# Kernel tuning notes

Measured on AMD Instinct MI355X. Metric: run time of the kernel, lower is better.

Reference implementation:

```python
import jax, jax.numpy as jnp
import numpy as np

IN_SHAPE = (8, 8, 8, 8)   # prod = 4096 in_features
OUT_SHAPE = (8, 8, 8, 8)  # prod = 4096 out_features
RANKS = (1, 64, 64, 64, 1)


def mpo2matrix(cores):
    # cores[k]: (r_k, i_k, o_k, r_{k+1}); contract the TT chain over rank axes.
    t = cores[0]
    for c in cores[1:]:
        t = jnp.tensordot(t, c, axes=([-1], [0]))
    # t: (1, i1,o1, i2,o2, i3,o3, i4,o4, 1) -> drop boundary ranks
    n = len(IN_SHAPE)
    io = tuple(d for p in zip(IN_SHAPE, OUT_SHAPE) for d in p)
    t = t.reshape(io)  # (i1,o1,...,in,on)
    perm = tuple(range(1, 2 * n, 2)) + tuple(range(0, 2 * n, 2))  # outputs first
    t = jnp.transpose(t, perm)
    return t.reshape(int(np.prod(OUT_SHAPE)), int(np.prod(IN_SHAPE)))  # (O, I)


def setup_inputs() -> dict:
    key = jax.random.key(0)
    ks = jax.random.split(key, 6)
    scale = 0.05  # keep reconstructed weight well-conditioned
    cores = []
    for i in range(4):
        r0, r1 = RANKS[i], RANKS[i + 1]
        cores.append(scale * jax.random.normal(ks[i], (r0, IN_SHAPE[i], OUT_SHAPE[i], r1), dtype=jnp.float32))
    x = jax.random.normal(ks[4], (8, 2048, 4096), dtype=jnp.float32)
    bias = jnp.zeros((4096,), dtype=jnp.float32)
    return {"x": x, "core0": cores[0], "core1": cores[1], "core2": cores[2], "core3": cores[3], "bias": bias}


def reference(x, core0, core1, core2, core3, bias):
    W = mpo2matrix([core0, core1, core2, core3])  # (O, I)
    res = x.reshape(-1, x.shape[-1])              # (B*S, I)
    out = res @ W.T + bias                        # F.linear
    return out.reshape(x.shape[:-1] + (-1,))
```

## Files before the change

### kernel.cpp

```cpp
#include <hip/hip_runtime.h>
#include <hip/hip_bf16.h>
#include <stdint.h>

typedef unsigned short u16;
typedef __attribute__((ext_vector_type(4))) float f32x4;
typedef __attribute__((ext_vector_type(8))) __bf16 bf16x8;

#define K_DIM 4096

__device__ __forceinline__ u16 f2bf_rne(float f) {
  union { float f; uint32_t u; } v; v.f = f;
  uint32_t u = v.u;
  return (u16)((u + 0x7fffu + ((u >> 16) & 1u)) >> 16);
}

__device__ __forceinline__ void gld_lds16(const u16* g, u16* l) {
  __builtin_amdgcn_global_load_lds((const __attribute__((address_space(1))) void*)g,
                                   (__attribute__((address_space(3))) void*)l,
                                   16, 0, 0);
}

__global__ __launch_bounds__(256) void k_cvt_x(const float* __restrict__ x, u16* __restrict__ xb, int n4) {
  const int stride = gridDim.x * 256;
  for (int i = blockIdx.x * 256 + threadIdx.x; i < n4; i += stride) {
    f32x4 a = ((const f32x4*)x)[i];
    uint2 o;
    o.x = (uint32_t)f2bf_rne(a[0]) | ((uint32_t)f2bf_rne(a[1]) << 16);
    o.y = (uint32_t)f2bf_rne(a[2]) | ((uint32_t)f2bf_rne(a[3]) << 16);
    ((uint2*)xb)[i] = o;
  }
}

__global__ __launch_bounds__(256) void k_t1(const float* __restrict__ c0, const float* __restrict__ c1,
                                            float* __restrict__ T1) {
  const int col = blockIdx.x * 256 + threadIdx.x;
  const int row = blockIdx.y;
  float acc = 0.f;
#pragma unroll 16
  for (int r = 0; r < 64; ++r) acc += c0[row * 64 + r] * c1[(size_t)r * 4096 + col];
  T1[(size_t)row * 4096 + col] = acc;
}

__global__ __launch_bounds__(256) void k_t2(const float* __restrict__ T1, const float* __restrict__ c2,
                                            float* __restrict__ T2) {
  __shared__ float t1s[16][64];
  const int tid = threadIdx.x;
  const int rowbase = blockIdx.y * 16;
  for (int idx = tid; idx < 1024; idx += 256)
    t1s[idx >> 6][idx & 63] = T1[(size_t)(rowbase + (idx >> 6)) * 64 + (idx & 63)];
  __syncthreads();
  const int col = blockIdx.x * 256 + tid;
  float acc[16];
#pragma unroll
  for (int j = 0; j < 16; ++j) acc[j] = 0.f;
  for (int r = 0; r < 64; ++r) {
    float b = c2[(size_t)r * 4096 + col];
#pragma unroll
    for (int j = 0; j < 16; ++j) acc[j] += t1s[j][r] * b;
  }
#pragma unroll
  for (int j = 0; j < 16; ++j) T2[(size_t)(rowbase + j) * 4096 + col] = acc[j];
}

__global__ __launch_bounds__(256) void k_w(const float* __restrict__ T2, const float* __restrict__ c3,
                                           u16* __restrict__ Wb) {
  __shared__ float t2p[64 * 65];
  __shared__ float c3t[64 * 64];
  const int tid = threadIdx.x;
  const int row12 = blockIdx.x;
  for (int idx = tid; idx < 4096; idx += 256) {
    t2p[(idx >> 6) * 65 + (idx & 63)] = T2[(size_t)row12 * 4096 + idx];
    const int r3 = idx >> 6, orow = idx & 63;
    c3t[r3 * 64 + ((orow & 7) << 3) + (orow >> 3)] = c3[idx];
  }
  __syncthreads();
  const int orow = tid >> 2;
  const int o3 = orow >> 3, o4 = orow & 7;
  const int ib16 = (tid & 3) * 16;
  const int rowA = ((ib16 >> 3)) * 8 + o3;
  const int rowB = ((ib16 >> 3) + 1) * 8 + o3;
  float acc[16];
#pragma unroll
  for (int c = 0; c < 16; ++c) acc[c] = 0.f;
  for (int r3 = 0; r3 < 64; ++r3) {
    const float ta = t2p[rowA * 65 + r3];
    const float tb = t2p[rowB * 65 + r3];
    const float* cv = &c3t[r3 * 64 + o4 * 8];
    f32x4 c0v = *(const f32x4*)cv;
    f32x4 c1v = *(const f32x4*)(cv + 4);
#pragma unroll
    for (int j = 0; j < 4; ++j) {
      acc[j]      += ta * c0v[j];
      acc[4 + j]  += ta * c1v[j];
      acc[8 + j]  += tb * c0v[j];
      acc[12 + j] += tb * c1v[j];
    }
  }
  const int i1o1 = row12 >> 6, i2o2 = row12 & 63;
  const int obase = ((i1o1 & 7) << 9) | ((i2o2 & 7) << 6);
  const int ibase = ((i1o1 >> 3) << 9) | ((i2o2 >> 3) << 6);
  uint32_t pk[8];
#pragma unroll
  for (int c = 0; c < 8; ++c)
    pk[c] = (uint32_t)f2bf_rne(acc[2 * c]) | ((uint32_t)f2bf_rne(acc[2 * c + 1]) << 16);
  uint4* dst = (uint4*)&Wb[(size_t)(obase + orow) * 4096 + ibase + ib16];
  dst[0] = make_uint4(pk[0], pk[1], pk[2], pk[3]);
  dst[1] = make_uint4(pk[4], pk[5], pk[6], pk[7]);
}

__global__ __launch_bounds__(512, 2) void k_gemm(const u16* __restrict__ Xb, const u16* __restrict__ Wb,
                                                 const float* __restrict__ bias, float* __restrict__ out) {
  __shared__ alignas(16) u16 Abuf[2][256 * 64];
  __shared__ alignas(16) u16 Bbuf[2][256 * 64];
  const int tid = threadIdx.x;
  const int wid = tid >> 6, l = tid & 63;
  const int bm = blockIdx.x;
  const int bn = blockIdx.y;
  const int wm = wid >> 2, wn = wid & 3;

  const int sch = (l & 7) ^ ((l >> 3) & 7);
  const int arow_g = 8 * wid + (l >> 3);
  const int brow_g = (wid >> 2) * 64 + 8 * (wid & 3) + (l >> 3);
  const u16* AgBase = Xb + (size_t)(bm * 256) * K_DIM + sch * 8;
  const u16* BgBase = Wb + (size_t)(bn * 256) * K_DIM + sch * 8;
  const int aldsw = (8 * wid) * 64;
  const int bldsw = ((wid >> 2) * 64 + 8 * (wid & 3)) * 64;

  const int kc0 = (((l >> 4)) ^ (l & 7)) * 8;
  const int kc1 = ((4 + (l >> 4)) ^ (l & 7)) * 8;
  const int aoff = (wm * 128 + (l & 15)) * 64;
  const int boff = (wn * 64 + (l & 15)) * 64;

  f32x4 acc[8][4];
#pragma unroll
  for (int m = 0; m < 8; ++m)
#pragma unroll
    for (int n = 0; n < 4; ++n) acc[m][n] = (f32x4){0.f, 0.f, 0.f, 0.f};

  bf16x8 a[4][2], b0[2][2], b1[2][2];

#define STAGE_A(T, S, PB) do { const size_t ko_ = (size_t)(T) * 64;                                  \
    gld_lds16(AgBase + (size_t)((S) * 64 + arow_g) * K_DIM + ko_,        &Abuf[PB][(S) * 4096 + aldsw]);        \
    gld_lds16(AgBase + (size_t)(128 + (S) * 64 + arow_g) * K_DIM + ko_,  &Abuf[PB][8192 + (S) * 4096 + aldsw]); \
  } while (0)
#define STAGE_B(T, S, PB) do { const size_t ko_ = (size_t)(T) * 64;                                  \
    gld_lds16(BgBase + (size_t)((S) * 32 + brow_g) * K_DIM + ko_,        &Bbuf[PB][(S) * 2048 + bldsw]);        \
    gld_lds16(BgBase + (size_t)(128 + (S) * 32 + brow_g) * K_DIM + ko_,  &Bbuf[PB][8192 + (S) * 2048 + bldsw]); \
  } while (0)

#define LDA(P, MH) do { _Pragma("unroll") for (int mt = 0; mt < 4; ++mt) {       \
    a[mt][0] = *(const bf16x8*)&Abuf[P][aoff + (MH) * 4096 + mt * 1024 + kc0];   \
    a[mt][1] = *(const bf16x8*)&Abuf[P][aoff + (MH) * 4096 + mt * 1024 + kc1]; } } while (0)
#define LDB(BV, P, NH) do { _Pragma("unroll") for (int nt = 0; nt < 2; ++nt) {   \
    BV[nt][0] = *(const bf16x8*)&Bbuf[P][boff + (NH) * 2048 + nt * 1024 + kc0];  \
    BV[nt][1] = *(const bf16x8*)&Bbuf[P][boff + (NH) * 2048 + nt * 1024 + kc1]; } } while (0)

#define MM(MB, NB, BV) do { __builtin_amdgcn_s_setprio(1);                                            \
    _Pragma("unroll") for (int mt = 0; mt < 4; ++mt)                                                  \
    _Pragma("unroll") for (int nt = 0; nt < 2; ++nt) {                                                \
      acc[(MB)+mt][(NB)+nt] = __builtin_amdgcn_mfma_f32_16x16x32_bf16(a[mt][0], BV[nt][0], acc[(MB)+mt][(NB)+nt], 0, 0, 0); \
      acc[(MB)+mt][(NB)+nt] = __builtin_amdgcn_mfma_f32_16x16x32_bf16(a[mt][1], BV[nt][1], acc[(MB)+mt][(NB)+nt], 0, 0, 0); } \
    __builtin_amdgcn_s_setprio(0); } while (0)

#define FENCE asm volatile("" ::: "memory")
#define BAR do { FENCE; __builtin_amdgcn_s_barrier(); FENCE; } while (0)
#define VMW4 asm volatile("s_waitcnt vmcnt(4)" ::: "memory")
#define VMW2 asm volatile("s_waitcnt vmcnt(2)" ::: "memory")
#define VMW0 asm volatile("s_waitcnt vmcnt(0)" ::: "memory")
#define LGKM asm volatile("s_waitcnt lgkmcnt(0)" ::: "memory")

#define TILE(T, P) do {                                                                          \
    LDA(P, 0); LDB(b0, P, 0); STAGE_A((T) + 1, 0, (P) ^ 1); BAR; LGKM; MM(0, 0, b0); VMW4; BAR;  \
    LDB(b1, P, 1);            STAGE_B((T) + 1, 0, (P) ^ 1); BAR; LGKM; MM(0, 2, b1); VMW4; BAR;  \
    LDA(P, 1);                STAGE_B((T) + 1, 1, (P) ^ 1); BAR; LGKM; MM(4, 2, b1); VMW4; BAR;  \
                              STAGE_A((T) + 1, 1, (P) ^ 1); BAR;       MM(4, 0, b0); VMW4; BAR;  \
  } while (0)

  STAGE_A(0, 0, 0); STAGE_B(0, 0, 0); STAGE_B(0, 1, 0); STAGE_A(0, 1, 0);
  VMW4; BAR;

#pragma unroll 1
  for (int t = 0; t < 62; t += 2) {
    TILE(t, 0);
    TILE(t + 1, 1);
  }
  TILE(62, 0);

  LDA(1, 0); LDB(b0, 1, 0); BAR; LGKM; MM(0, 0, b0); VMW2; BAR;
  LDB(b1, 1, 1);            BAR; LGKM; MM(0, 2, b1); VMW0; BAR;
  LDA(1, 1);                BAR; LGKM; MM(4, 2, b1); BAR;
                                       MM(4, 0, b0);

  const int orow_base = bm * 256 + wm * 128 + (l >> 4) * 4;
  const int ocol_base = bn * 256 + wn * 64 + (l & 15);
#pragma unroll
  for (int n = 0; n < 4; ++n) {
    const int oc = ocol_base + n * 16;
    const float bv = bias[oc];
#pragma unroll
    for (int m = 0; m < 8; ++m) {
      const int orb = orow_base + m * 16;
#pragma unroll
      for (int j = 0; j < 4; ++j)
        out[(size_t)(orb + j) * 4096 + oc] = acc[m][n][j] + bv;
    }
  }
#undef STAGE_A
#undef STAGE_B
#undef LDA
#undef LDB
#undef MM
#undef FENCE
#undef BAR
#undef VMW4
#undef VMW2
#undef VMW0
#undef LGKM
#undef TILE
}

extern "C" void kernel_launch(void* const* d_in, const int* in_sizes, int n_in,
                              void* d_out, int out_size, void* d_ws, size_t ws_size,
                              hipStream_t stream) {
  const float* x    = (const float*)d_in[0];
  const float* c0   = (const float*)d_in[1];
  const float* c1   = (const float*)d_in[2];
  const float* c2   = (const float*)d_in[3];
  const float* c3   = (const float*)d_in[4];
  const float* bias = (const float*)d_in[5];
  float* out = (float*)d_out;

  char* ws = (char*)d_ws;
  float* T1 = (float*)ws;
  float* T2 = (float*)(ws + (1u << 20));
  u16*   Wb = (u16*)(ws + (1u << 20) + (64u << 20));
  u16*   Xb = (u16*)(ws + (1u << 20) + (64u << 20) + (32u << 20));

  hipLaunchKernelGGL(k_cvt_x, dim3(2048), dim3(256), 0, stream, x, Xb, 16777216);
  hipLaunchKernelGGL(k_t1,    dim3(16, 64), dim3(256), 0, stream, c0, c1, T1);
  hipLaunchKernelGGL(k_t2,    dim3(16, 256), dim3(256), 0, stream, T1, c2, T2);
  hipLaunchKernelGGL(k_w,     dim3(4096), dim3(256), 0, stream, T2, c3, Wb);
  hipLaunchKernelGGL(k_gemm,  dim3(64, 16), dim3(512), 0, stream, Xb, Wb, bias, out);
}
```

Before: 1.020 ms.

## Deepen GEMM global-to-LDS prefetch to two tiles ahead

```diff
diff --git a/kernel.cpp b/kernel.cpp
--- a/kernel.cpp
+++ b/kernel.cpp
@@ -164,31 +164,34 @@
 
 #define FENCE asm volatile("" ::: "memory")
 #define BAR do { FENCE; __builtin_amdgcn_s_barrier(); FENCE; } while (0)
-#define VMW4 asm volatile("s_waitcnt vmcnt(4)" ::: "memory")
-#define VMW2 asm volatile("s_waitcnt vmcnt(2)" ::: "memory")
-#define VMW0 asm volatile("s_waitcnt vmcnt(0)" ::: "memory")
-#define LGKM asm volatile("s_waitcnt lgkmcnt(0)" ::: "memory")
-
-#define TILE(T, P) do {                                                                          \
-    LDA(P, 0); LDB(b0, P, 0); STAGE_A((T) + 1, 0, (P) ^ 1); BAR; LGKM; MM(0, 0, b0); VMW4; BAR;  \
-    LDB(b1, P, 1);            STAGE_B((T) + 1, 0, (P) ^ 1); BAR; LGKM; MM(0, 2, b1); VMW4; BAR;  \
-    LDA(P, 1);                STAGE_B((T) + 1, 1, (P) ^ 1); BAR; LGKM; MM(4, 2, b1); VMW4; BAR;  \
-                              STAGE_A((T) + 1, 1, (P) ^ 1); BAR;       MM(4, 0, b0); VMW4; BAR;  \
+#define VMW(N) asm volatile("s_waitcnt vmcnt(" #N ")" ::: "memory")
+#define LGKM do { asm volatile("s_waitcnt lgkmcnt(0)" ::: "memory"); \
+    __builtin_amdgcn_sched_barrier(0); } while (0)
+
+#define TILE(T, P) do {                                                                              \
+    LDA(P, 0); LDB(b0, P, 0);                                 BAR; LGKM; MM(0, 0, b0); VMW(10); BAR; \
+    LDB(b1, P, 1); STAGE_A((T)+2, 0, P); STAGE_B((T)+2, 0, P); BAR; LGKM; MM(0, 2, b1); VMW(12); BAR; \
+    LDA(P, 1); STAGE_B((T)+2, 1, P);                          BAR; LGKM; MM(4, 2, b1);          BAR; \
+    STAGE_A((T)+2, 1, P);                                     BAR;       MM(4, 0, b0); VMW(12); BAR; \
   } while (0)
 
   STAGE_A(0, 0, 0); STAGE_B(0, 0, 0); STAGE_B(0, 1, 0); STAGE_A(0, 1, 0);
-  VMW4; BAR;
+  STAGE_A(1, 0, 1); STAGE_B(1, 0, 1); STAGE_B(1, 1, 1); STAGE_A(1, 1, 1);
+  VMW(12); BAR;
 
 #pragma unroll 1
   for (int t = 0; t < 62; t += 2) {
     TILE(t, 0);
     TILE(t + 1, 1);
   }
-  TILE(62, 0);
-
-  LDA(1, 0); LDB(b0, 1, 0); BAR; LGKM; MM(0, 0, b0); VMW2; BAR;
-  LDB(b1, 1, 1);            BAR; LGKM; MM(0, 2, b1); VMW0; BAR;
-  LDA(1, 1);                BAR; LGKM; MM(4, 2, b1); BAR;
+
+  LDA(0, 0); LDB(b0, 0, 0); BAR; LGKM; MM(0, 0, b0); VMW(10); BAR;
+  LDB(b1, 0, 1);            BAR; LGKM; MM(0, 2, b1); VMW(8);  BAR;
+  LDA(0, 1);                BAR; LGKM; MM(4, 2, b1);          BAR;
+                            BAR;       MM(4, 0, b0); VMW(4);  BAR;
+  LDA(1, 0); LDB(b0, 1, 0); BAR; LGKM; MM(0, 0, b0); VMW(2); BAR;
+  LDB(b1, 1, 1);            BAR; LGKM; MM(0, 2, b1); VMW(0); BAR;
+  LDA(1, 1);                BAR; LGKM; MM(4, 2, b1);         BAR;
                                        MM(4, 0, b0);
 
   const int orow_base = bm * 256 + wm * 128 + (l >> 4) * 4;
@@ -212,9 +215,7 @@
 #undef MM
 #undef FENCE
 #undef BAR
-#undef VMW4
-#undef VMW2
-#undef VMW0
+#undef VMW
 #undef LGKM
 #undef TILE
 }
```

Result: slower. 1.044 ms (+2.4%).
